# Optimization experiments

Hardware: AMD Instinct MI355X
Metric: run time of the kernel (lower is better)

Reference implementation:

```python
import jax, jax.numpy as jnp
import numpy as np

N_NODES = 50000
IN_F = 128
OUT_F = 128
N_EDGES = 800000
ALPHA = 0.2  # LeakyReLU negative slope
EPS = 1e-16

def _xavier(key, shape, gain=1.414):
    fan_in, fan_out = shape[0], shape[1]
    bound = gain * np.sqrt(6.0 / (fan_in + fan_out))
    return jax.random.uniform(key, shape, jnp.float32, -bound, bound)

def setup_inputs() -> dict:
    key = jax.random.key(0)
    k_h, k_e, k_W, k_a = jax.random.split(key, 4)
    h = jax.random.normal(k_h, (N_NODES, IN_F), dtype=jnp.float32)
    edge_index = jax.random.randint(k_e, (2, N_EDGES), 0, N_NODES, dtype=jnp.int64)
    W = _xavier(k_W, (IN_F, OUT_F))
    a = _xavier(k_a, (2 * OUT_F, 1))
    return {"h": h, "edge_index": edge_index, "W": W, "a": a}

def reference(h, edge_index, W, a):
    # h: [N, F_in], edge_index: [2, E], W: [F_in, F_out], a: [2*F_out, 1]
    Wh = h @ W                                   # [N, F_out]
    row, col = edge_index[0], edge_index[1]
    # cat([Wh_i, Wh_j]) @ a  ==  Wh_i @ a1 + Wh_j @ a2  (compute per-node, gather per-edge)
    a1, a2 = a[:OUT_F, 0], a[OUT_F:, 0]
    s1 = Wh @ a1                                 # [N]
    s2 = Wh @ a2                                 # [N]
    e = jax.nn.leaky_relu(s1[row] + s2[col], negative_slope=ALPHA)  # [E]
    # NOTE: original code's "e_rowmax" is actually a segment SUM (index_add_), replicated faithfully
    e_rowsum = jax.ops.segment_sum(e, row, num_segments=N_NODES)    # [N]
    e_exp = jnp.exp(e - e_rowsum[row])                              # [E]
    e_exp_sum = jax.ops.segment_sum(e_exp, row, num_segments=N_NODES)
    attention = e_exp / (e_exp_sum[row] + EPS)                      # [E]
    # weighted scatter-add aggregation
    h_prime = jax.ops.segment_sum(attention[:, None] * Wh[col], row, num_segments=N_NODES)
    return h_prime
```

## Files before the change

kernel.cpp:

```cpp
#include <hip/hip_runtime.h>
#include <hip/hip_bf16.h>
#include <math.h>

#define NNODES 50000
#define NF 128
#define NEDGES 800000
#define ALPHA 0.2f
#define EPS 1e-16f
#define EPT 4
#define GEMM_BLOCKS 782
#define EDGE_BLOCKS 782
#define CAP 64

typedef __attribute__((ext_vector_type(8))) short bf16x8;
typedef __attribute__((ext_vector_type(4))) float f32x4;

__device__ inline unsigned bf16rne(float x) {
    unsigned u = __float_as_uint(x);
    return (u + 0x7FFFu + ((u >> 16) & 1u)) >> 16;
}
__device__ inline float bflo(unsigned u) { return __uint_as_float(u << 16); }
__device__ inline float bfhi(unsigned u) { return __uint_as_float(u & 0xFFFF0000u); }

__global__ __launch_bounds__(256) void prep(const float* __restrict__ W,
                                            const float* __restrict__ a,
                                            ushort* __restrict__ WbF,
                                            float* __restrict__ Wa1,
                                            float* __restrict__ Wa2,
                                            int* __restrict__ count) {
    if (blockIdx.x < 8) {
        int s = blockIdx.x * 256 + threadIdx.x;
        int l = s & 63;
        int ct = (s >> 6) & 7;
        int ks = s >> 9;
        int c = ct * 16 + (l & 15);
        int g = l >> 4;
        ushort v[8];
        #pragma unroll
        for (int j = 0; j < 8; ++j) {
            int k = ks * 32 + ((j >> 2) << 4) + g * 4 + (j & 3);
            v[j] = (ushort)bf16rne(W[k * NF + c]);
        }
        *(uint4*)&WbF[(size_t)s * 8] = *(uint4*)v;
    } else if (blockIdx.x == 8) {
        int k = threadIdx.x;
        if (k < NF) {
            float t1 = 0.f, t2 = 0.f;
            for (int c = 0; c < NF; ++c) {
                float w = W[k * NF + c];
                t1 += w * a[c];
                t2 += w * a[NF + c];
            }
            Wa1[k] = t1;
            Wa2[k] = t2;
        }
    } else {
        const int stride = (gridDim.x - 9) * 256;
        for (int i = (blockIdx.x - 9) * 256 + threadIdx.x; i < NNODES; i += stride)
            count[i] = 0;
    }
}

__global__ __launch_bounds__(256) void gemm_scatter(const float* __restrict__ h,
                                                    const ushort* __restrict__ WbF,
                                                    const float* __restrict__ Wa1,
                                                    const float* __restrict__ Wa2,
                                                    const int* __restrict__ ei,
                                                    ushort* __restrict__ WhBu,
                                                    float* __restrict__ s1,
                                                    float* __restrict__ s2,
                                                    int* __restrict__ count,
                                                    int* __restrict__ colbucket) {
    __shared__ ushort ldsB[16384];
    const int tid = threadIdx.x;

    if (blockIdx.x < EDGE_BLOCKS) {
        const int base = blockIdx.x * 256 + tid;
        const int stride = EDGE_BLOCKS * 256;
        int r[EPT], c[EPT];
        #pragma unroll
        for (int k = 0; k < EPT; ++k) {
            int idx = base + k * stride;
            if (idx < NEDGES) {
                r[k] = ei[idx];
                c[k] = ei[NEDGES + idx];
            } else r[k] = -1;
        }
        int rk[EPT];
        #pragma unroll
        for (int k = 0; k < EPT; ++k)
            if (r[k] >= 0) rk[k] = atomicAdd(&count[r[k]], 1);
        #pragma unroll
        for (int k = 0; k < EPT; ++k)
            if (r[k] >= 0 && rk[k] < CAP)
                colbucket[r[k] * CAP + rk[k]] = c[k];
        return;
    }

    const int bid = blockIdx.x - EDGE_BLOCKS;

    #pragma unroll
    for (int i = 0; i < 8; ++i) {
        int off8 = (tid + i * 256) * 8;
        *(uint4*)&ldsB[off8] = *(const uint4*)&WbF[off8];
    }
    __syncthreads();

    const int lane = tid & 63;
    const int wrow = tid >> 6;
    const int m = lane & 15;
    const int g = lane >> 4;
    const int row = bid * 64 + wrow * 16 + m;
    const int rowc = (row < NNODES) ? row : 0;

    f32x4 acc[8];
    #pragma unroll
    for (int t = 0; t < 8; ++t) acc[t] = (f32x4){0.f, 0.f, 0.f, 0.f};

    float p1 = 0.f, p2 = 0.f;
    #pragma unroll
    for (int ks = 0; ks < 4; ++ks) {
        const float4 ha = *(const float4*)&h[(size_t)rowc * NF + ks * 32 + g * 4];
        const float4 hb = *(const float4*)&h[(size_t)rowc * NF + ks * 32 + 16 + g * 4];
        const float4 wa1a = *(const float4*)&Wa1[ks * 32 + g * 4];
        const float4 wa1b = *(const float4*)&Wa1[ks * 32 + 16 + g * 4];
        const float4 wa2a = *(const float4*)&Wa2[ks * 32 + g * 4];
        const float4 wa2b = *(const float4*)&Wa2[ks * 32 + 16 + g * 4];
        p1 += ha.x * wa1a.x + ha.y * wa1a.y + ha.z * wa1a.z + ha.w * wa1a.w
            + hb.x * wa1b.x + hb.y * wa1b.y + hb.z * wa1b.z + hb.w * wa1b.w;
        p2 += ha.x * wa2a.x + ha.y * wa2a.y + ha.z * wa2a.z + ha.w * wa2a.w
            + hb.x * wa2b.x + hb.y * wa2b.y + hb.z * wa2b.z + hb.w * wa2b.w;
        bf16x8 afrag;
        afrag[0] = (short)bf16rne(ha.x);
        afrag[1] = (short)bf16rne(ha.y);
        afrag[2] = (short)bf16rne(ha.z);
        afrag[3] = (short)bf16rne(ha.w);
        afrag[4] = (short)bf16rne(hb.x);
        afrag[5] = (short)bf16rne(hb.y);
        afrag[6] = (short)bf16rne(hb.z);
        afrag[7] = (short)bf16rne(hb.w);
        #pragma unroll
        for (int ct = 0; ct < 8; ++ct) {
            bf16x8 bfrag = *(bf16x8*)&ldsB[((ks * 8 + ct) * 64 + lane) * 8];
            acc[ct] = __builtin_amdgcn_mfma_f32_16x16x32_bf16(afrag, bfrag, acc[ct], 0, 0, 0);
        }
    }

    p1 += __shfl_xor(p1, 16); p1 += __shfl_xor(p1, 32);
    p2 += __shfl_xor(p2, 16); p2 += __shfl_xor(p2, 32);
    if (g == 0 && row < NNODES) { s1[row] = p1; s2[row] = p2; }

    const int orow = bid * 64 + wrow * 16 + g * 4;
    #pragma unroll
    for (int r = 0; r < 4; ++r) {
        int gr = orow + r;
        if (gr < NNODES) {
            #pragma unroll
            for (int ct = 0; ct < 8; ++ct)
                WhBu[(size_t)gr * NF + ct * 16 + m] = (ushort)bf16rne(acc[ct][r]);
        }
    }
}

__global__ __launch_bounds__(256) void aggregate(const int* __restrict__ count,
                                                 const int* __restrict__ colbucket,
                                                 const float* __restrict__ s1,
                                                 const float* __restrict__ s2,
                                                 const unsigned* __restrict__ WhB,
                                                 float* __restrict__ out) {
    const int wid = threadIdx.x >> 6;
    const int lane = threadIdx.x & 63;
    const int row = blockIdx.x * 4 + wid;
    if (row >= NNODES) return;
    const int deg = min(count[row], CAP);

    int cv = 0;
    float ev = 0.f;
    if (lane < deg) cv = colbucket[row * CAP + lane];
    const float s1r = s1[row];
    if (lane < deg) {
        float s = s1r + s2[cv];
        ev = (s >= 0.f) ? s : ALPHA * s;
    }

    float rs = ev;
    #pragma unroll
    for (int off = 32; off; off >>= 1) rs += __shfl_xor(rs, off);
    float xv = (lane < deg) ? expf(ev - rs) : 0.f;
    float ds = xv;
    #pragma unroll
    for (int off = 32; off; off >>= 1) ds += __shfl_xor(ds, off);
    const float invd = 1.0f / (ds + EPS);

    float accx = 0.f, accy = 0.f;
    int j = 0;
    for (; j + 8 <= deg; j += 8) {
        int cc[8]; unsigned u[8]; float ww[8];
        #pragma unroll
        for (int k = 0; k < 8; ++k) cc[k] = __shfl(cv, j + k);
        #pragma unroll
        for (int k = 0; k < 8; ++k) u[k] = WhB[(size_t)cc[k] * 64 + lane];
        #pragma unroll
        for (int k = 0; k < 8; ++k) ww[k] = __shfl(xv, j + k);
        #pragma unroll
        for (int k = 0; k < 8; ++k) {
            float w = ww[k] * invd;
            accx += w * bflo(u[k]);
            accy += w * bfhi(u[k]);
        }
    }
    for (; j < deg; ++j) {
        int c = __shfl(cv, j);
        unsigned u = WhB[(size_t)c * 64 + lane];
        float w = __shfl(xv, j) * invd;
        accx += w * bflo(u);
        accy += w * bfhi(u);
    }
    ((float2*)out)[(size_t)row * 64 + lane] = make_float2(accx, accy);
}

extern "C" void kernel_launch(void* const* d_in, const int* in_sizes, int n_in,
                              void* d_out, int out_size, void* d_ws, size_t ws_size,
                              hipStream_t stream) {
    const float* h  = (const float*)d_in[0];
    const int*   ei = (const int*)d_in[1];
    const float* W  = (const float*)d_in[2];
    const float* a  = (const float*)d_in[3];
    float* out = (float*)d_out;

    char* ws = (char*)d_ws;
    size_t off = 0;
    auto alloc = [&](size_t bytes) -> void* {
        void* p = ws + off;
        off += (bytes + 255) & ~(size_t)255;
        return p;
    };

    unsigned* WhB       = (unsigned*)alloc((size_t)NNODES * 64 * 4);
    int*      colbucket = (int*)alloc((size_t)NNODES * CAP * 4);
    ushort*   WbF       = (ushort*)alloc((size_t)2048 * 16);
    float*    Wa1       = (float*)alloc((size_t)NF * 4);
    float*    Wa2       = (float*)alloc((size_t)NF * 4);
    int*      count     = (int*)alloc((size_t)NNODES * 4);
    float*    s1        = (float*)alloc((size_t)NNODES * 4);
    float*    s2        = (float*)alloc((size_t)NNODES * 4);

    prep<<<58, 256, 0, stream>>>(W, a, WbF, Wa1, Wa2, count);
    gemm_scatter<<<EDGE_BLOCKS + GEMM_BLOCKS, 256, 0, stream>>>(
        h, WbF, Wa1, Wa2, ei, (ushort*)WhB, s1, s2, count, colbucket);
    aggregate<<<(NNODES + 3) / 4, 256, 0, stream>>>(count, colbucket, s1, s2, WhB, out);
}
```

Before: 98.00 us.

## Replace global-atomic edge bucketing with chunked LDS histogram, scan, and scatter

Edge bucketing no longer uses global atomicAdd on per-row counters. It becomes a three-step counting sort: per-chunk byte-packed histograms built in LDS, a column scan over chunks that gives per-row offsets and counts, and a scatter pass that ranks edges with LDS atomics. Column indices are stored as ushort to halve bucket traffic. The change removes contended global atomics but adds two kernel launches and about 12.8 MB of histogram traffic. Byte-packed counters and ushort columns assume per-row degree below 256 and node ids below 65536.

```diff
diff --git a/kernel.cpp b/kernel.cpp
--- a/kernel.cpp
+++ b/kernel.cpp
@@ -7,9 +7,10 @@
 #define NEDGES 800000
 #define ALPHA 0.2f
 #define EPS 1e-16f
-#define EPT 4
 #define GEMM_BLOCKS 782
-#define EDGE_BLOCKS 782
+#define NCHUNK 128
+#define ECHUNK 6250
+#define NHW 12500
 #define CAP 64
 
 typedef __attribute__((ext_vector_type(8))) short bf16x8;
@@ -26,8 +27,7 @@
                                             const float* __restrict__ a,
                                             ushort* __restrict__ WbF,
                                             float* __restrict__ Wa1,
-                                            float* __restrict__ Wa2,
-                                            int* __restrict__ count) {
+                                            float* __restrict__ Wa2) {
     if (blockIdx.x < 8) {
         int s = blockIdx.x * 256 + threadIdx.x;
         int l = s & 63;
@@ -42,7 +42,7 @@
             v[j] = (ushort)bf16rne(W[k * NF + c]);
         }
         *(uint4*)&WbF[(size_t)s * 8] = *(uint4*)v;
-    } else if (blockIdx.x == 8) {
+    } else {
         int k = threadIdx.x;
         if (k < NF) {
             float t1 = 0.f, t2 = 0.f;
@@ -54,50 +54,38 @@
             Wa1[k] = t1;
             Wa2[k] = t2;
         }
-    } else {
-        const int stride = (gridDim.x - 9) * 256;
-        for (int i = (blockIdx.x - 9) * 256 + threadIdx.x; i < NNODES; i += stride)
-            count[i] = 0;
-    }
-}
-
-__global__ __launch_bounds__(256) void gemm_scatter(const float* __restrict__ h,
-                                                    const ushort* __restrict__ WbF,
-                                                    const float* __restrict__ Wa1,
-                                                    const float* __restrict__ Wa2,
-                                                    const int* __restrict__ ei,
-                                                    ushort* __restrict__ WhBu,
-                                                    float* __restrict__ s1,
-                                                    float* __restrict__ s2,
-                                                    int* __restrict__ count,
-                                                    int* __restrict__ colbucket) {
-    __shared__ ushort ldsB[16384];
+    }
+}
+
+__global__ __launch_bounds__(256) void gemm_hist(const float* __restrict__ h,
+                                                 const ushort* __restrict__ WbF,
+                                                 const float* __restrict__ Wa1,
+                                                 const float* __restrict__ Wa2,
+                                                 const int* __restrict__ ei,
+                                                 ushort* __restrict__ WhBu,
+                                                 float* __restrict__ s1,
+                                                 float* __restrict__ s2,
+                                                 unsigned char* __restrict__ H) {
+    __shared__ char lds[NHW * 4];
     const int tid = threadIdx.x;
 
-    if (blockIdx.x < EDGE_BLOCKS) {
-        const int base = blockIdx.x * 256 + tid;
-        const int stride = EDGE_BLOCKS * 256;
-        int r[EPT], c[EPT];
-        #pragma unroll
-        for (int k = 0; k < EPT; ++k) {
-            int idx = base + k * stride;
-            if (idx < NEDGES) {
-                r[k] = ei[idx];
-                c[k] = ei[NEDGES + idx];
-            } else r[k] = -1;
-        }
-        int rk[EPT];
-        #pragma unroll
-        for (int k = 0; k < EPT; ++k)
-            if (r[k] >= 0) rk[k] = atomicAdd(&count[r[k]], 1);
-        #pragma unroll
-        for (int k = 0; k < EPT; ++k)
-            if (r[k] >= 0 && rk[k] < CAP)
-                colbucket[r[k] * CAP + rk[k]] = c[k];
+    if (blockIdx.x < NCHUNK) {
+        unsigned* hist = (unsigned*)lds;
+        for (int i = tid; i < NHW; i += 256) hist[i] = 0u;
+        __syncthreads();
+        const int e0 = blockIdx.x * ECHUNK;
+        for (int i = tid; i < ECHUNK; i += 256) {
+            int r = ei[e0 + i];
+            atomicAdd(&hist[r >> 2], 1u << (8 * (r & 3)));
+        }
+        __syncthreads();
+        unsigned* Hc = (unsigned*)&H[(size_t)blockIdx.x * NNODES];
+        for (int i = tid; i < NHW; i += 256) Hc[i] = hist[i];
         return;
     }
 
-    const int bid = blockIdx.x - EDGE_BLOCKS;
+    const int bid = blockIdx.x - NCHUNK;
+    ushort* ldsB = (ushort*)lds;
 
     #pragma unroll
     for (int i = 0; i < 8; ++i) {
@@ -162,8 +150,46 @@
     }
 }
 
+__global__ __launch_bounds__(256) void scan_chunks(const unsigned char* __restrict__ H,
+                                                   unsigned char* __restrict__ B,
+                                                   int* __restrict__ count) {
+    const int gid = blockIdx.x * 256 + threadIdx.x;
+    const int r0 = gid * 4;
+    if (r0 >= NNODES) return;
+    unsigned run = 0u;
+    for (int c = 0; c < NCHUNK; ++c) {
+        unsigned hv = *(const unsigned*)&H[(size_t)c * NNODES + r0];
+        *(unsigned*)&B[(size_t)c * NNODES + r0] = run;
+        run += hv;
+    }
+    count[r0 + 0] = run & 0xFF;
+    count[r0 + 1] = (run >> 8) & 0xFF;
+    count[r0 + 2] = (run >> 16) & 0xFF;
+    count[r0 + 3] = (run >> 24) & 0xFF;
+}
+
+__global__ __launch_bounds__(256) void scatter(const int* __restrict__ ei,
+                                               const unsigned char* __restrict__ B,
+                                               ushort* __restrict__ bucket) {
+    __shared__ unsigned hist[NHW];
+    const int tid = threadIdx.x;
+    for (int i = tid; i < NHW; i += 256) hist[i] = 0u;
+    __syncthreads();
+    const int e0 = blockIdx.x * ECHUNK;
+    const unsigned char* Bc = &B[(size_t)blockIdx.x * NNODES];
+    for (int i = tid; i < ECHUNK; i += 256) {
+        int r = ei[e0 + i];
+        int col = ei[NEDGES + e0 + i];
+        unsigned old = atomicAdd(&hist[r >> 2], 1u << (8 * (r & 3)));
+        int lrank = (old >> (8 * (r & 3))) & 0xFF;
+        int pos = (int)Bc[r] + lrank;
+        if (pos < CAP)
+            bucket[r * CAP + pos] = (ushort)col;
+    }
+}
+
 __global__ __launch_bounds__(256) void aggregate(const int* __restrict__ count,
-                                                 const int* __restrict__ colbucket,
+                                                 const ushort* __restrict__ colbucket,
                                                  const float* __restrict__ s1,
                                                  const float* __restrict__ s2,
                                                  const unsigned* __restrict__ WhB,
@@ -176,7 +202,7 @@
 
     int cv = 0;
     float ev = 0.f;
-    if (lane < deg) cv = colbucket[row * CAP + lane];
+    if (lane < deg) cv = (int)colbucket[row * CAP + lane];
     const float s1r = s1[row];
     if (lane < deg) {
         float s = s1r + s2[cv];
@@ -236,17 +262,21 @@
         return p;
     };
 
-    unsigned* WhB       = (unsigned*)alloc((size_t)NNODES * 64 * 4);
-    int*      colbucket = (int*)alloc((size_t)NNODES * CAP * 4);
-    ushort*   WbF       = (ushort*)alloc((size_t)2048 * 16);
-    float*    Wa1       = (float*)alloc((size_t)NF * 4);
-    float*    Wa2       = (float*)alloc((size_t)NF * 4);
-    int*      count     = (int*)alloc((size_t)NNODES * 4);
-    float*    s1        = (float*)alloc((size_t)NNODES * 4);
-    float*    s2        = (float*)alloc((size_t)NNODES * 4);
-
-    prep<<<58, 256, 0, stream>>>(W, a, WbF, Wa1, Wa2, count);
-    gemm_scatter<<<EDGE_BLOCKS + GEMM_BLOCKS, 256, 0, stream>>>(
-        h, WbF, Wa1, Wa2, ei, (ushort*)WhB, s1, s2, count, colbucket);
-    aggregate<<<(NNODES + 3) / 4, 256, 0, stream>>>(count, colbucket, s1, s2, WhB, out);
-}
+    unsigned*      WhB    = (unsigned*)alloc((size_t)NNODES * 64 * 4);
+    ushort*        bucket = (ushort*)alloc((size_t)NNODES * CAP * 2);
+    unsigned char* H      = (unsigned char*)alloc((size_t)NCHUNK * NNODES);
+    unsigned char* B      = (unsigned char*)alloc((size_t)NCHUNK * NNODES);
+    ushort*        WbF    = (ushort*)alloc((size_t)2048 * 16);
+    float*         Wa1    = (float*)alloc((size_t)NF * 4);
+    float*         Wa2    = (float*)alloc((size_t)NF * 4);
+    int*           count  = (int*)alloc((size_t)NNODES * 4);
+    float*         s1     = (float*)alloc((size_t)NNODES * 4);
+    float*         s2     = (float*)alloc((size_t)NNODES * 4);
+
+    prep<<<9, 256, 0, stream>>>(W, a, WbF, Wa1, Wa2);
+    gemm_hist<<<NCHUNK + GEMM_BLOCKS, 256, 0, stream>>>(
+        h, WbF, Wa1, Wa2, ei, (ushort*)WhB, s1, s2, H);
+    scan_chunks<<<49, 256, 0, stream>>>(H, B, count);
+    scatter<<<NCHUNK, 256, 0, stream>>>(ei, B, bucket);
+    aggregate<<<(NNODES + 3) / 4, 256, 0, stream>>>(count, bucket, s1, s2, WhB, out);
+}
```

Result: no change. 99.10 us (+1.1%).
